# Kernel optimization log

Measured on AMD Instinct MI355X. Metric: run time of the kernel, lower is better.

The kernel has to match this reference:

```python
import jax, jax.numpy as jnp
import numpy as np

H = 1024  # hidden_size == embedding_size


def setup_inputs() -> dict:
    key = jax.random.key(0)
    ks = jax.random.split(key, 14)
    B, T, L, V = 2, 1, 8192, 50000
    emb_table = jax.random.normal(ks[0], (V, H), jnp.float32)
    emb_table = emb_table.at[0].set(0.0)  # row 0 zeroed as in the torch module
    return {
        "input_ids": jax.random.randint(ks[1], (B, T), 0, V),
        "last_context": jax.random.normal(ks[2], (B, T, H), jnp.float32),
        "last_hidden": jax.random.normal(ks[3], (1, B, H), jnp.float32),
        "encoder_outputs": jax.random.normal(ks[4], (B, L, H), jnp.float32),
        "emb_table": emb_table,
        "w_ih": jax.random.normal(ks[5], (3 * H, 2 * H), jnp.float32) * 0.02,
        "w_hh": jax.random.normal(ks[6], (3 * H, H), jnp.float32) * 0.02,
        "b_ih": jax.random.normal(ks[7], (3 * H,), jnp.float32) * 0.02,
        "b_hh": jax.random.normal(ks[8], (3 * H,), jnp.float32) * 0.02,
        "attn_w": jax.random.normal(ks[9], (H, 2 * H), jnp.float32) * 0.02,
        "attn_b": jax.random.normal(ks[10], (H,), jnp.float32) * 0.02,
        "v": jax.random.normal(ks[11], (H,), jnp.float32),
        "out_w": jax.random.normal(ks[12], (50000, 2 * H), jnp.float32) * 0.02,
        "out_b": jax.random.normal(ks[13], (50000,), jnp.float32) * 0.02,
    }


def _forward(input_ids, last_context, last_hidden, encoder_outputs, emb_table,
             w_ih, w_hh, b_ih, b_hh, attn_w, attn_b, v, out_w, out_b):
    # Embedding lookup (dropout p=0 -> identity)
    embedded = emb_table[input_ids]                      # [B,1,H]
    rnn_in = jnp.concatenate([embedded, last_context], -1)  # [B,1,2H]

    # Single-step, single-layer GRU (torch gate order: r, z, n)
    x = rnn_in[:, 0]                                     # [B,2H]
    h = last_hidden[0]                                   # [B,H]
    gx = x @ w_ih.T + b_ih                               # [B,3H]
    gh = h @ w_hh.T + b_hh                               # [B,3H]
    r = jax.nn.sigmoid(gx[:, :H] + gh[:, :H])
    z = jax.nn.sigmoid(gx[:, H:2 * H] + gh[:, H:2 * H])
    n = jnp.tanh(gx[:, 2 * H:] + r * gh[:, 2 * H:])
    h_new = (1.0 - z) * n + z * h                        # [B,H]
    rnn_output = h_new[:, None, :]                       # [B,1,H]
    hidden = h_new[None]                                 # [1,B,H]

    # Bahdanau 'concat' attention, vectorized over the seq_len loop:
    # energy[b,i] = v . (attn_w @ concat(h_new[b], enc[b,i]) + attn_b)
    w_h, w_e = attn_w[:, :H], attn_w[:, H:]
    e_h = h_new @ w_h.T + attn_b                         # [B,H]
    e_e = jnp.einsum('blh,kh->blk', encoder_outputs, w_e)  # [B,L,H]
    energies = jnp.einsum('blk,k->bl', e_e + e_h[:, None, :], v)  # [B,L]
    attn_weights = jax.nn.softmax(energies, axis=1)      # [B,L]
    context = jnp.einsum('bl,blh->bh', attn_weights, encoder_outputs)[:, None, :]  # [B,1,H]

    # Output projection over concat(rnn_output, context)
    cat = jnp.concatenate([rnn_output, context], -1)     # [B,1,2H]
    output = cat @ out_w.T + out_b                       # [B,1,V]
    return output, context, hidden, embedded, rnn_output


def reference(input_ids, last_context, last_hidden, encoder_outputs, emb_table,
              w_ih, w_hh, b_ih, b_hh, attn_w, attn_b, v, out_w, out_b):
    return _forward(input_ids, last_context, last_hidden, encoder_outputs, emb_table,
                    w_ih, w_hh, b_ih, b_hh, attn_w, attn_b, v, out_w, out_b)
```

## Files before the change

kernel.cpp:

```cpp
#include <hip/hip_runtime.h>

#define H 1024
#define LEN 8192
#define V 50000
#define NTILE 12500

__device__ __forceinline__ float dot4(float4 a, float4 b) {
    return a.x * b.x + a.y * b.y + a.z * b.z + a.w * b.w;
}

__device__ __forceinline__ void gld_lds16(const float* g, float* l) {
    __builtin_amdgcn_global_load_lds(
        (const __attribute__((address_space(1))) void*)g,
        (__attribute__((address_space(3))) void*)l, 16, 0, 0);
}

__global__ void k_u(const float* __restrict__ attn_w,
                    const float* __restrict__ v,
                    float* __restrict__ u) {
    __shared__ float red[16][16];
    int bid = blockIdx.x;
    int t   = threadIdx.x;
    int kg  = t >> 4;
    int hi  = t & 15;
    int h   = bid * 16 + hi;
    float acc = 0.f;
#pragma unroll 8
    for (int i = 0; i < 64; ++i) {
        int k = kg * 64 + i;
        acc += v[k] * attn_w[(long)k * (2 * H) + H + h];
    }
    red[kg][hi] = acc;
    __syncthreads();
    if (t < 16) {
        float s = 0.f;
#pragma unroll
        for (int g = 0; g < 16; ++g) s += red[g][t];
        u[bid * 16 + t] = s;
    }
}

__global__ void k_big(const int* __restrict__ ids,
                      const float* __restrict__ emb,
                      const float* __restrict__ lctx,
                      const float* __restrict__ lhid,
                      const float* __restrict__ w_ih,
                      const float* __restrict__ w_hh,
                      const float* __restrict__ b_ih,
                      const float* __restrict__ b_hh,
                      const float* __restrict__ enc,
                      const float* __restrict__ u,
                      float* __restrict__ o_hidden,
                      float* __restrict__ o_rnn,
                      float* __restrict__ out_emb,
                      float* __restrict__ en) {
    __shared__ float lds[3][4][4];
    int bid = blockIdx.x;
    int t   = threadIdx.x;

    if (bid < 4096) {
        int row  = (bid << 2) + (t >> 6);
        int lane = t & 63;
        const float* e = enc + (long)row * H;
        float acc = 0.f;
#pragma unroll
        for (int c = 0; c < 4; ++c) {
            int k = c * 256 + lane * 4;
            float4 ev = *(const float4*)(e + k);
            float4 uv = *(const float4*)(u + k);
            acc += dot4(ev, uv);
        }
        for (int off = 32; off; off >>= 1) acc += __shfl_down(acc, off, 64);
        if (lane == 0) en[row] = acc;
        return;
    }
    if (bid < 4104) {
        int idx = (bid - 4096) * 256 + t;
        int b = idx >> 10, h = idx & 1023;
        out_emb[idx] = emb[(long)ids[b] * H + h];
        return;
    }

    int hh = bid - 4104;
    int kb = t * 8;

    float4 x0a, x0b, x1a, x1b;
    if (kb < H) {
        const float* p0 = emb + (long)ids[0] * H + kb;
        const float* p1 = emb + (long)ids[1] * H + kb;
        x0a = *(const float4*)p0;       x0b = *(const float4*)(p0 + 4);
        x1a = *(const float4*)p1;       x1b = *(const float4*)(p1 + 4);
    } else {
        const float* p0 = lctx + (kb - H);
        const float* p1 = lctx + H + (kb - H);
        x0a = *(const float4*)p0;       x0b = *(const float4*)(p0 + 4);
        x1a = *(const float4*)p1;       x1b = *(const float4*)(p1 + 4);
    }
    int kb2 = t * 4;
    float4 h0 = *(const float4*)(lhid + kb2);
    float4 h1 = *(const float4*)(lhid + H + kb2);

    for (int g = 0; g < 3; ++g) {
        const float* wi = w_ih + ((long)g * H + hh) * (2 * H) + kb;
        const float* wh = w_hh + ((long)g * H + hh) * H + kb2;
        float4 wa = *(const float4*)wi;
        float4 wb = *(const float4*)(wi + 4);
        float4 wc = *(const float4*)wh;
        float a0 = dot4(wa, x0a) + dot4(wb, x0b);
        float a1 = dot4(wa, x1a) + dot4(wb, x1b);
        float c0 = dot4(wc, h0);
        float c1 = dot4(wc, h1);
        for (int off = 32; off; off >>= 1) {
            a0 += __shfl_down(a0, off, 64);
            a1 += __shfl_down(a1, off, 64);
            c0 += __shfl_down(c0, off, 64);
            c1 += __shfl_down(c1, off, 64);
        }
        if ((t & 63) == 0) {
            int w = t >> 6;
            lds[g][w][0] = a0; lds[g][w][1] = a1;
            lds[g][w][2] = c0; lds[g][w][3] = c1;
        }
    }
    __syncthreads();
    if (t == 0) {
        float gx[3][2], gh[3][2];
        for (int g = 0; g < 3; ++g) {
            float s0 = 0, s1 = 0, s2 = 0, s3 = 0;
            for (int w = 0; w < 4; ++w) {
                s0 += lds[g][w][0]; s1 += lds[g][w][1];
                s2 += lds[g][w][2]; s3 += lds[g][w][3];
            }
            float bi = b_ih[g * H + hh], bh = b_hh[g * H + hh];
            gx[g][0] = s0 + bi; gx[g][1] = s1 + bi;
            gh[g][0] = s2 + bh; gh[g][1] = s3 + bh;
        }
        for (int b = 0; b < 2; ++b) {
            float r  = 1.f / (1.f + expf(-(gx[0][b] + gh[0][b])));
            float z  = 1.f / (1.f + expf(-(gx[1][b] + gh[1][b])));
            float n  = tanhf(gx[2][b] + r * gh[2][b]);
            float hp = lhid[b * H + hh];
            float hn = (1.f - z) * n + z * hp;
            o_hidden[b * H + hh] = hn;
            o_rnn[b * H + hh]    = hn;
        }
    }
}

__global__ void k_ctx(const float* __restrict__ enc,
                      const float* __restrict__ en,
                      float* __restrict__ part) {
    int b  = blockIdx.x >> 8;
    int lc = blockIdx.x & 255;
    int t  = threadIdx.x;
    const float* e_row = en + b * LEN;

    __shared__ float red[4];
    __shared__ float wlds[32];

    float m = -3.4e38f;
#pragma unroll 8
    for (int i = t; i < LEN; i += 256) m = fmaxf(m, e_row[i]);
    for (int off = 32; off; off >>= 1) m = fmaxf(m, __shfl_xor(m, off, 64));
    if ((t & 63) == 0) red[t >> 6] = m;
    __syncthreads();
    m = fmaxf(fmaxf(red[0], red[1]), fmaxf(red[2], red[3]));

    float s = 0.f;
#pragma unroll 8
    for (int i = t; i < LEN; i += 256) s += expf(e_row[i] - m);
    for (int off = 32; off; off >>= 1) s += __shfl_xor(s, off, 64);
    __syncthreads();
    if ((t & 63) == 0) red[t >> 6] = s;
    __syncthreads();
    float inv = 1.f / (red[0] + red[1] + red[2] + red[3]);

    if (t < 32) wlds[t] = expf(e_row[lc * 32 + t] - m) * inv;
    __syncthreads();

    const float* e = enc + ((long)b * LEN + lc * 32) * H + t * 4;
    float4 acc = {0.f, 0.f, 0.f, 0.f};
#pragma unroll 8
    for (int i = 0; i < 32; ++i) {
        float w = wlds[i];
        float4 ev = *(const float4*)(e + (long)i * H);
        acc.x += w * ev.x; acc.y += w * ev.y; acc.z += w * ev.z; acc.w += w * ev.w;
    }
    *(float4*)(part + (long)blockIdx.x * H + t * 4) = acc;
}

__global__ void k_ctx_red(const float* __restrict__ part,
                          float* __restrict__ out_ctx) {
    __shared__ float red[8][32];
    int t   = threadIdx.x;
    int il  = t & 31;
    int grp = t >> 5;
    int idx = blockIdx.x * 32 + il;
    int b = idx >> 10, h = idx & 1023;
    const float* p = part + (long)(b << 8) * H + h;
    float acc = 0.f;
#pragma unroll 8
    for (int i = 0; i < 32; ++i) acc += p[(long)(grp * 32 + i) * H];
    red[grp][il] = acc;
    __syncthreads();
    if (t < 32) {
        float s = 0.f;
#pragma unroll
        for (int g = 0; g < 8; ++g) s += red[g][t];
        out_ctx[blockIdx.x * 32 + t] = s;
    }
}

__global__ void __launch_bounds__(256)
k_out(const float* __restrict__ ow,
      const float* __restrict__ ob,
      const float* __restrict__ hnew,
      const float* __restrict__ ctx,
      float* __restrict__ out) {
    __shared__ float cat[2][2 * H];
    __shared__ float wt[2][4 * 2 * H];
    int t    = threadIdx.x;
    int lane = t & 63;
    int wv   = t >> 6;

    {
        float4* c0 = (float4*)cat[0];
        float4* c1 = (float4*)cat[1];
#pragma unroll
        for (int r = 0; r < 2; ++r) {
            int idx = t + r * 256;
            int k   = idx * 4;
            if (k < H) {
                c0[idx] = *(const float4*)(hnew + k);
                c1[idx] = *(const float4*)(hnew + H + k);
            } else {
                c0[idx] = *(const float4*)(ctx + (k - H));
                c1[idx] = *(const float4*)(ctx + H + (k - H));
            }
        }
    }

    {
        const float* src = ow + (long)blockIdx.x * (4 * 2 * H);
#pragma unroll
        for (int i = 0; i < 8; ++i)
            gld_lds16(src + i * 1024 + t * 4, wt[0] + i * 1024 + t * 4);
    }
    __syncthreads();

    const float4* c0 = (const float4*)cat[0];
    const float4* c1 = (const float4*)cat[1];
    int buf = 0;
    for (int T = blockIdx.x; T < NTILE; T += 512) {
        int Tn = T + 512;
        if (Tn < NTILE) {
            const float* src = ow + (long)Tn * (4 * 2 * H);
            float* dst = wt[buf ^ 1];
#pragma unroll
            for (int i = 0; i < 8; ++i)
                gld_lds16(src + i * 1024 + t * 4, dst + i * 1024 + t * 4);
        }
        const float4* wr = (const float4*)(wt[buf] + wv * (2 * H));
        float a0 = 0.f, a1 = 0.f;
#pragma unroll
        for (int j = 0; j < 8; ++j) {
            float4 w = wr[lane + 64 * j];
            a0 += dot4(w, c0[lane + 64 * j]);
            a1 += dot4(w, c1[lane + 64 * j]);
        }
        for (int off = 32; off; off >>= 1) {
            a0 += __shfl_down(a0, off, 64);
            a1 += __shfl_down(a1, off, 64);
        }
        if (lane == 0) {
            long row = (long)T * 4 + wv;
            float bb = ob[row];
            out[row]     = a0 + bb;
            out[V + row] = a1 + bb;
        }
        __syncthreads();
        buf ^= 1;
    }
}

extern "C" void kernel_launch(void* const* d_in, const int* in_sizes, int n_in,
                              void* d_out, int out_size, void* d_ws, size_t ws_size,
                              hipStream_t stream) {
    const int*   ids    = (const int*)  d_in[0];
    const float* lctx   = (const float*)d_in[1];
    const float* lhid   = (const float*)d_in[2];
    const float* enc    = (const float*)d_in[3];
    const float* emb    = (const float*)d_in[4];
    const float* w_ih   = (const float*)d_in[5];
    const float* w_hh   = (const float*)d_in[6];
    const float* b_ih   = (const float*)d_in[7];
    const float* b_hh   = (const float*)d_in[8];
    const float* attn_w = (const float*)d_in[9];
    const float* v      = (const float*)d_in[11];
    const float* out_w  = (const float*)d_in[12];
    const float* out_b  = (const float*)d_in[13];

    float* out_f       = (float*)d_out;
    float* o_output    = out_f;
    float* o_context   = out_f + 100000;
    float* o_hidden    = out_f + 102048;
    float* o_embedded  = out_f + 104096;
    float* o_rnn       = out_f + 106144;

    float* ws   = (float*)d_ws;
    float* U    = ws;
    float* EN   = ws + 1024;
    float* PART = ws + 17408;

    k_u      <<<64,   256, 0, stream>>>(attn_w, v, U);
    k_big    <<<5128, 256, 0, stream>>>(ids, emb, lctx, lhid, w_ih, w_hh,
                                        b_ih, b_hh, enc, U,
                                        o_hidden, o_rnn, o_embedded, EN);
    k_ctx    <<<512,  256, 0, stream>>>(enc, EN, PART);
    k_ctx_red<<<64,   256, 0, stream>>>(PART, o_context);
    k_out    <<<512,  256, 0, stream>>>(out_w, out_b, o_hidden, o_context,
                                        o_output);
}
```

Before: 123.2 us.

## Fuse attention energy, softmax and context into single-pass online-softmax kernel

Replaces the separate energy pass and context pass over encoder_outputs with one kernel. Each block stages 8 encoder rows in LDS, computes their energies, and forms a local max, exp-sum and weighted partial vector. A reduction kernel then rescales the partials flash-attention style. The u projection and the GRU/embedding work are merged into one launch, cutting a launch and one full read of the 64MB encoder tensor, at the cost of a much larger partial buffer (2048x1024 floats) that the reducer must read.

```diff
diff --git a/kernel.cpp b/kernel.cpp
--- a/kernel.cpp
+++ b/kernel.cpp
@@ -4,6 +4,8 @@
 #define LEN 8192
 #define V 50000
 #define NTILE 12500
+#define CHUNK 8
+#define NCH (LEN / CHUNK)
 
 __device__ __forceinline__ float dot4(float4 a, float4 b) {
     return a.x * b.x + a.y * b.y + a.z * b.z + a.w * b.w;
@@ -15,73 +17,53 @@
         (__attribute__((address_space(3))) void*)l, 16, 0, 0);
 }
 
-__global__ void k_u(const float* __restrict__ attn_w,
-                    const float* __restrict__ v,
-                    float* __restrict__ u) {
-    __shared__ float red[16][16];
-    int bid = blockIdx.x;
-    int t   = threadIdx.x;
-    int kg  = t >> 4;
-    int hi  = t & 15;
-    int h   = bid * 16 + hi;
-    float acc = 0.f;
-#pragma unroll 8
-    for (int i = 0; i < 64; ++i) {
-        int k = kg * 64 + i;
-        acc += v[k] * attn_w[(long)k * (2 * H) + H + h];
-    }
-    red[kg][hi] = acc;
-    __syncthreads();
-    if (t < 16) {
-        float s = 0.f;
-#pragma unroll
-        for (int g = 0; g < 16; ++g) s += red[g][t];
-        u[bid * 16 + t] = s;
-    }
-}
-
-__global__ void k_big(const int* __restrict__ ids,
+__global__ void k_pre(const float* __restrict__ attn_w,
+                      const float* __restrict__ v,
+                      float* __restrict__ u,
+                      const int* __restrict__ ids,
                       const float* __restrict__ emb,
+                      float* __restrict__ out_emb,
                       const float* __restrict__ lctx,
                       const float* __restrict__ lhid,
                       const float* __restrict__ w_ih,
                       const float* __restrict__ w_hh,
                       const float* __restrict__ b_ih,
                       const float* __restrict__ b_hh,
-                      const float* __restrict__ enc,
-                      const float* __restrict__ u,
                       float* __restrict__ o_hidden,
-                      float* __restrict__ o_rnn,
-                      float* __restrict__ out_emb,
-                      float* __restrict__ en) {
+                      float* __restrict__ o_rnn) {
+    __shared__ float red[16][16];
     __shared__ float lds[3][4][4];
     int bid = blockIdx.x;
     int t   = threadIdx.x;
 
-    if (bid < 4096) {
-        int row  = (bid << 2) + (t >> 6);
-        int lane = t & 63;
-        const float* e = enc + (long)row * H;
+    if (bid < 64) {
+        int kg = t >> 4;
+        int hi = t & 15;
+        int h  = bid * 16 + hi;
         float acc = 0.f;
-#pragma unroll
-        for (int c = 0; c < 4; ++c) {
-            int k = c * 256 + lane * 4;
-            float4 ev = *(const float4*)(e + k);
-            float4 uv = *(const float4*)(u + k);
-            acc += dot4(ev, uv);
-        }
-        for (int off = 32; off; off >>= 1) acc += __shfl_down(acc, off, 64);
-        if (lane == 0) en[row] = acc;
+#pragma unroll 8
+        for (int i = 0; i < 64; ++i) {
+            int k = kg * 64 + i;
+            acc += v[k] * attn_w[(long)k * (2 * H) + H + h];
+        }
+        red[kg][hi] = acc;
+        __syncthreads();
+        if (t < 16) {
+            float s = 0.f;
+#pragma unroll
+            for (int g = 0; g < 16; ++g) s += red[g][t];
+            u[bid * 16 + t] = s;
+        }
         return;
     }
-    if (bid < 4104) {
-        int idx = (bid - 4096) * 256 + t;
+    if (bid < 72) {
+        int idx = (bid - 64) * 256 + t;
         int b = idx >> 10, h = idx & 1023;
         out_emb[idx] = emb[(long)ids[b] * H + h];
         return;
     }
 
-    int hh = bid - 4104;
+    int hh = bid - 72;
     int kb = t * 8;
 
     float4 x0a, x0b, x1a, x1b;
@@ -147,67 +129,111 @@
     }
 }
 
-__global__ void k_ctx(const float* __restrict__ enc,
-                      const float* __restrict__ en,
-                      float* __restrict__ part) {
-    int b  = blockIdx.x >> 8;
-    int lc = blockIdx.x & 255;
+__global__ void __launch_bounds__(256)
+k_ctx(const float* __restrict__ enc,
+      const float* __restrict__ u,
+      float* __restrict__ pvec,
+      float* __restrict__ marr,
+      float* __restrict__ sarr) {
+    __shared__ float erow[CHUNK * H];
+    __shared__ float elds[CHUNK];
+    int t    = threadIdx.x;
+    int lane = t & 63;
+    int wv   = t >> 6;
+    int b    = blockIdx.x >> 10;
+    int ch   = blockIdx.x & 1023;
+
+    const float* src = enc + ((long)b * LEN + (long)ch * CHUNK) * H;
+#pragma unroll
+    for (int i = 0; i < CHUNK; ++i)
+        gld_lds16(src + i * H + t * 4, erow + i * H + t * 4);
+
+    float4 uf[4];
+#pragma unroll
+    for (int c = 0; c < 4; ++c)
+        uf[c] = *(const float4*)(u + c * 256 + lane * 4);
+
+    __syncthreads();
+
+#pragma unroll
+    for (int rr = 0; rr < 2; ++rr) {
+        int r = wv * 2 + rr;
+        float acc = 0.f;
+#pragma unroll
+        for (int c = 0; c < 4; ++c) {
+            float4 ev = *(const float4*)(erow + r * H + c * 256 + lane * 4);
+            acc += dot4(ev, uf[c]);
+        }
+        for (int off = 32; off; off >>= 1) acc += __shfl_down(acc, off, 64);
+        if (lane == 0) elds[r] = acc;
+    }
+    __syncthreads();
+
+    float m = elds[0];
+#pragma unroll
+    for (int r = 1; r < CHUNK; ++r) m = fmaxf(m, elds[r]);
+    float p[CHUNK];
+    float s = 0.f;
+#pragma unroll
+    for (int r = 0; r < CHUNK; ++r) { p[r] = expf(elds[r] - m); s += p[r]; }
+
+    float4 acc = {0.f, 0.f, 0.f, 0.f};
+#pragma unroll
+    for (int r = 0; r < CHUNK; ++r) {
+        float4 ev = *(const float4*)(erow + r * H + t * 4);
+        acc.x += p[r] * ev.x; acc.y += p[r] * ev.y;
+        acc.z += p[r] * ev.z; acc.w += p[r] * ev.w;
+    }
+    *(float4*)(pvec + (long)blockIdx.x * H + t * 4) = acc;
+    if (t == 0) { marr[blockIdx.x] = m; sarr[blockIdx.x] = s; }
+}
+
+__global__ void __launch_bounds__(256)
+k_red(const float* __restrict__ pvec,
+      const float* __restrict__ marr,
+      const float* __restrict__ sarr,
+      float* __restrict__ out_ctx) {
+    __shared__ float scale[NCH];
+    __shared__ float red[8][32];
     int t  = threadIdx.x;
-    const float* e_row = en + b * LEN;
-
-    __shared__ float red[4];
-    __shared__ float wlds[32];
+    int b  = blockIdx.x >> 5;
+    int h0 = (blockIdx.x & 31) * 32;
+    const float* mb = marr + b * NCH;
+    const float* sb = sarr + b * NCH;
 
     float m = -3.4e38f;
-#pragma unroll 8
-    for (int i = t; i < LEN; i += 256) m = fmaxf(m, e_row[i]);
+    for (int i = t; i < NCH; i += 256) m = fmaxf(m, mb[i]);
     for (int off = 32; off; off >>= 1) m = fmaxf(m, __shfl_xor(m, off, 64));
-    if ((t & 63) == 0) red[t >> 6] = m;
-    __syncthreads();
-    m = fmaxf(fmaxf(red[0], red[1]), fmaxf(red[2], red[3]));
-
-    float s = 0.f;
-#pragma unroll 8
-    for (int i = t; i < LEN; i += 256) s += expf(e_row[i] - m);
-    for (int off = 32; off; off >>= 1) s += __shfl_xor(s, off, 64);
-    __syncthreads();
-    if ((t & 63) == 0) red[t >> 6] = s;
-    __syncthreads();
-    float inv = 1.f / (red[0] + red[1] + red[2] + red[3]);
-
-    if (t < 32) wlds[t] = expf(e_row[lc * 32 + t] - m) * inv;
-    __syncthreads();
-
-    const float* e = enc + ((long)b * LEN + lc * 32) * H + t * 4;
-    float4 acc = {0.f, 0.f, 0.f, 0.f};
-#pragma unroll 8
-    for (int i = 0; i < 32; ++i) {
-        float w = wlds[i];
-        float4 ev = *(const float4*)(e + (long)i * H);
-        acc.x += w * ev.x; acc.y += w * ev.y; acc.z += w * ev.z; acc.w += w * ev.w;
-    }
-    *(float4*)(part + (long)blockIdx.x * H + t * 4) = acc;
-}
-
-__global__ void k_ctx_red(const float* __restrict__ part,
-                          float* __restrict__ out_ctx) {
-    __shared__ float red[8][32];
-    int t   = threadIdx.x;
-    int il  = t & 31;
-    int grp = t >> 5;
-    int idx = blockIdx.x * 32 + il;
-    int b = idx >> 10, h = idx & 1023;
-    const float* p = part + (long)(b << 8) * H + h;
+    if ((t & 63) == 0) red[0][t >> 6] = m;
+    __syncthreads();
+    m = fmaxf(fmaxf(red[0][0], red[0][1]), fmaxf(red[0][2], red[0][3]));
+    __syncthreads();
+
+    float d = 0.f;
+    for (int i = t; i < NCH; i += 256) {
+        float sc = expf(mb[i] - m);
+        scale[i] = sc;
+        d += sc * sb[i];
+    }
+    for (int off = 32; off; off >>= 1) d += __shfl_xor(d, off, 64);
+    if ((t & 63) == 0) red[0][t >> 6] = d;
+    __syncthreads();
+    float inv = 1.f / (red[0][0] + red[0][1] + red[0][2] + red[0][3]);
+    __syncthreads();
+
+    int grp = t >> 5, il = t & 31;
+    const float* pv = pvec + (long)b * NCH * H + (h0 + il);
     float acc = 0.f;
-#pragma unroll 8
-    for (int i = 0; i < 32; ++i) acc += p[(long)(grp * 32 + i) * H];
+#pragma unroll 4
+    for (int c = grp * 128; c < grp * 128 + 128; ++c)
+        acc += scale[c] * pv[(long)c * H];
     red[grp][il] = acc;
     __syncthreads();
     if (t < 32) {
-        float s = 0.f;
-#pragma unroll
-        for (int g = 0; g < 8; ++g) s += red[g][t];
-        out_ctx[blockIdx.x * 32 + t] = s;
+        float ssum = 0.f;
+#pragma unroll
+        for (int g = 0; g < 8; ++g) ssum += red[g][t];
+        out_ctx[b * H + h0 + t] = ssum * inv;
     }
 }
 
@@ -239,7 +265,6 @@
             }
         }
     }
-
     {
         const float* src = ow + (long)blockIdx.x * (4 * 2 * H);
 #pragma unroll
@@ -309,15 +334,15 @@
 
     float* ws   = (float*)d_ws;
     float* U    = ws;
-    float* EN   = ws + 1024;
-    float* PART = ws + 17408;
-
-    k_u      <<<64,   256, 0, stream>>>(attn_w, v, U);
-    k_big    <<<5128, 256, 0, stream>>>(ids, emb, lctx, lhid, w_ih, w_hh,
-                                        b_ih, b_hh, enc, U,
-                                        o_hidden, o_rnn, o_embedded, EN);
-    k_ctx    <<<512,  256, 0, stream>>>(enc, EN, PART);
-    k_ctx_red<<<64,   256, 0, stream>>>(PART, o_context);
-    k_out    <<<512,  256, 0, stream>>>(out_w, out_b, o_hidden, o_context,
-                                        o_output);
-}
+    float* MARR = ws + 1024;
+    float* SARR = ws + 3072;
+    float* PVEC = ws + 5120;
+
+    k_pre<<<1096, 256, 0, stream>>>(attn_w, v, U, ids, emb, o_embedded,
+                                    lctx, lhid, w_ih, w_hh, b_ih, b_hh,
+                                    o_hidden, o_rnn);
+    k_ctx<<<2048, 256, 0, stream>>>(enc, U, PVEC, MARR, SARR);
+    k_red<<<64,   256, 0, stream>>>(PVEC, MARR, SARR, o_context);
+    k_out<<<512,  256, 0, stream>>>(out_w, out_b, o_hidden, o_context,
+                                    o_output);
+}
```

Result: faster. 115.7 us (-6.1%).
